# Kernel optimization log

Hardware: AMD Instinct MI355X
Metric: run time of the kernel (lower is better)

## Reference

```python
import jax, jax.numpy as jnp
import numpy as np
import math

B, S, D = 16, 2048, 64


def setup_inputs() -> dict:
    key = jax.random.key(0)
    k1, k2, k3 = jax.random.split(key, 3)
    Q = jax.random.normal(k1, (B, S, D), dtype=jnp.float32)
    K = jax.random.normal(k2, (B, S, D), dtype=jnp.float32)
    V = jax.random.normal(k3, (B, S, D), dtype=jnp.float32)
    # causal mask: True where attention is disallowed (strict upper triangle)
    mask = jnp.triu(jnp.ones((S, S), dtype=bool), k=1)
    mask = jnp.broadcast_to(mask, (B, S, S))
    return {"Q": Q, "K": K, "V": V, "mask": mask, "dk": 64}


def reference(Q, K, V, mask, dk):
    # w = Q K^T / sqrt(dk), masked fill with -1e8
    w = jnp.einsum("bqd,bkd->bqk", Q, K) / math.sqrt(dk)
    w = jnp.where(mask, jnp.float32(-1.0e8), w)
    # distance_func in the original returns 0 (constant, under no_grad),
    # so exp(-1e8 * 0) * w == w; output is softmax of masked scaled scores.
    distance_score = jnp.float32(0.0)
    s = jnp.exp(jnp.float32(-1.0e8) * distance_score) * w
    a = jax.nn.softmax(s, axis=-1)
    return a
```

## Files before the change

### kernel.cpp

```cpp
#include <hip/hip_runtime.h>

using bf16x8 = __attribute__((ext_vector_type(8))) short;
using u16x8  = __attribute__((ext_vector_type(8))) unsigned short;
using u32x4  = __attribute__((ext_vector_type(4))) unsigned;
using f32x4  = __attribute__((ext_vector_type(4))) float;

static constexpr int S  = 2048;
static constexpr int D  = 64;
static constexpr int TQ = 64;
static constexpr float QSCALE = 0.18033688f;

__device__ __forceinline__ unsigned cvtpk(float lo, float hi) {
    unsigned r;
    asm("v_cvt_pk_bf16_f32 %0, %1, %2" : "=v"(r) : "v"(lo), "v"(hi));
    return r;
}
__device__ __forceinline__ f32x4 mfma16(bf16x8 a, bf16x8 b, f32x4 c) {
    return __builtin_amdgcn_mfma_f32_16x16x32_bf16(a, b, c, 0, 0, 0);
}
__device__ __forceinline__ void lbar() {
    asm volatile("s_waitcnt lgkmcnt(0)" ::: "memory");
    __builtin_amdgcn_s_barrier();
    asm volatile("" ::: "memory");
}

__global__ __launch_bounds__(256, 2)
void monotonic_attn(const float* __restrict__ Qg, const float* __restrict__ Kg,
                    float* __restrict__ out)
{
    __shared__ unsigned short qlds[4096];
    __shared__ unsigned short kls[4][2][1024];
    __shared__ float red[4][64];

    const int bid  = blockIdx.x;
    const int xcd  = bid & 7;
    const int m    = bid >> 3;
    const int bloc = (m < 32) ? 0 : 1;
    const int qt   = (m < 32) ? (31 - m) : (m - 32);
    const int b    = 2 * xcd + bloc;

    const int tid = threadIdx.x, lane = tid & 63, wv = tid >> 6;
    const int l15 = lane & 15, g = lane >> 4;

    const float* __restrict__ Qb = Qg + (size_t)b * S * D;
    const float* __restrict__ Kb = Kg + (size_t)b * S * D;
    float* __restrict__ outb = out + (size_t)b * (size_t)S * S;

    const int q0   = qt * TQ;
    const int kend = q0 + TQ;
    const int nC   = kend >> 4;
    const int ni   = (nC - wv + 3) >> 2;

    const int srow  = lane >> 2;
    const int scp   = lane & 3;
    const int woff0 = srow * 64 + (((scp << 1)    ) ^ (srow & 7)) * 8;
    const int woff1 = srow * 64 + (((scp << 1) | 1) ^ (srow & 7)) * 8;
    const int roff0 = l15 * 64 + ((g    ) ^ (l15 & 7)) * 8;
    const int roff1 = l15 * 64 + ((4 | g) ^ (l15 & 7)) * 8;

    {
        const int qrow = tid >> 2, qc = tid & 3;
        const float4* src = reinterpret_cast<const float4*>(Qb + (size_t)(q0 + qrow) * D + qc * 16);
        float v[16];
        *reinterpret_cast<float4*>(&v[0])  = src[0];
        *reinterpret_cast<float4*>(&v[4])  = src[1];
        *reinterpret_cast<float4*>(&v[8])  = src[2];
        *reinterpret_cast<float4*>(&v[12]) = src[3];
        #pragma unroll
        for (int j = 0; j < 2; ++j) {
            u32x4 w;
            #pragma unroll
            for (int p = 0; p < 4; ++p)
                w[p] = cvtpk(v[8 * j + 2 * p] * QSCALE, v[8 * j + 2 * p + 1] * QSCALE);
            const int chunk = qc * 2 + j;
            const int off = qrow * 64 + (chunk ^ (qrow & 7)) * 8;
            *reinterpret_cast<u32x4*>(&qlds[off]) = w;
        }
    }
    lbar();

    bf16x8 qf[4][2];
    #pragma unroll
    for (int qs = 0; qs < 4; ++qs) {
        const int row = qs * 16 + l15;
        #pragma unroll
        for (int c = 0; c < 2; ++c) {
            const int off = row * 64 + ((((c << 2) | g)) ^ (row & 7)) * 8;
            qf[qs][c] = *reinterpret_cast<const bf16x8*>(&qlds[off]);
        }
    }

    float inv4[4];
    for (int pass = 0; pass < 2; ++pass) {
        float rsum[4] = {0.f, 0.f, 0.f, 0.f};

        float4 ra0, ra1, ra2, ra3, rb0, rb1, rb2, rb3;
        auto issueA = [&](int i) {
            const float4* p4 = reinterpret_cast<const float4*>(Kb) + ((wv + 4 * i) << 8) + (lane << 2);
            ra0 = p4[0]; ra1 = p4[1]; ra2 = p4[2]; ra3 = p4[3];
        };
        auto issueB = [&](int i) {
            const float4* p4 = reinterpret_cast<const float4*>(Kb) + ((wv + 4 * i) << 8) + (lane << 2);
            rb0 = p4[0]; rb1 = p4[1]; rb2 = p4[2]; rb3 = p4[3];
        };
        auto stage = [&](int i, const float4& x0, const float4& x1,
                         const float4& x2, const float4& x3) {
            u32x4 w0, w1;
            w0[0] = cvtpk(x0.x, x0.y); w0[1] = cvtpk(x0.z, x0.w);
            w0[2] = cvtpk(x1.x, x1.y); w0[3] = cvtpk(x1.z, x1.w);
            w1[0] = cvtpk(x2.x, x2.y); w1[1] = cvtpk(x2.z, x2.w);
            w1[2] = cvtpk(x3.x, x3.y); w1[3] = cvtpk(x3.z, x3.w);
            unsigned short* bp = &kls[wv][i & 1][0];
            *reinterpret_cast<u32x4*>(&bp[woff0]) = w0;
            *reinterpret_cast<u32x4*>(&bp[woff1]) = w1;
        };
        auto comp = [&](int i) {
            const unsigned short* bp = &kls[wv][i & 1][0];
            const bf16x8 kf0 = *reinterpret_cast<const bf16x8*>(&bp[roff0]);
            const bf16x8 kf1 = *reinterpret_cast<const bf16x8*>(&bp[roff1]);
            const int klo = (wv + 4 * i) << 4;
            const int kb  = klo + g * 4;
            #pragma unroll
            for (int qs = 0; qs < 4; ++qs) {
                const int qmin = q0 + qs * 16, qg = qmin + l15;
                if (pass == 0) {
                    if (klo > qmin + 15) continue;
                    f32x4 acc = {0.f, 0.f, 0.f, 0.f};
                    acc = mfma16(kf0, qf[qs][0], acc);
                    acc = mfma16(kf1, qf[qs][1], acc);
                    if (klo + 15 <= qmin) {
                        rsum[qs] += exp2f(acc[0]) + exp2f(acc[1]) + exp2f(acc[2]) + exp2f(acc[3]);
                    } else {
                        #pragma unroll
                        for (int r = 0; r < 4; ++r)
                            rsum[qs] += (kb + r <= qg) ? exp2f(acc[r]) : 0.f;
                    }
                } else {
                    f32x4 ov = {0.f, 0.f, 0.f, 0.f};
                    if (klo <= qmin + 15) {
                        f32x4 acc = {0.f, 0.f, 0.f, 0.f};
                        acc = mfma16(kf0, qf[qs][0], acc);
                        acc = mfma16(kf1, qf[qs][1], acc);
                        if (klo + 15 <= qmin) {
                            ov[0] = exp2f(acc[0]) * inv4[qs];
                            ov[1] = exp2f(acc[1]) * inv4[qs];
                            ov[2] = exp2f(acc[2]) * inv4[qs];
                            ov[3] = exp2f(acc[3]) * inv4[qs];
                        } else {
                            ov[0] = (kb + 0 <= qg) ? exp2f(acc[0]) * inv4[qs] : 0.f;
                            ov[1] = (kb + 1 <= qg) ? exp2f(acc[1]) * inv4[qs] : 0.f;
                            ov[2] = (kb + 2 <= qg) ? exp2f(acc[2]) * inv4[qs] : 0.f;
                            ov[3] = (kb + 3 <= qg) ? exp2f(acc[3]) * inv4[qs] : 0.f;
                        }
                    }
                    *reinterpret_cast<f32x4*>(outb + (size_t)qg * S + kb) = ov;
                }
            }
        };

        if (ni > 0) issueA(0);
        if (ni > 1) issueB(1);
        int i = 0;
        for (; i + 2 <= ni; i += 2) {
            stage(i, ra0, ra1, ra2, ra3);
            if (i + 2 < ni) issueA(i + 2);
            comp(i);
            stage(i + 1, rb0, rb1, rb2, rb3);
            if (i + 3 < ni) issueB(i + 3);
            comp(i + 1);
        }
        if (i < ni) { stage(i, ra0, ra1, ra2, ra3); comp(i); }

        if (pass == 0) {
            #pragma unroll
            for (int qs = 0; qs < 4; ++qs) {
                float v = rsum[qs];
                v += __shfl_xor(v, 16);
                v += __shfl_xor(v, 32);
                if (g == 0) red[wv][qs * 16 + l15] = v;
            }
            lbar();
            #pragma unroll
            for (int qs = 0; qs < 4; ++qs) {
                const int qi = qs * 16 + l15;
                inv4[qs] = 1.f / (red[0][qi] + red[1][qi] + red[2][qi] + red[3][qi]);
            }
        }
    }

    {
        f32x4 z = {0.f, 0.f, 0.f, 0.f};
        const size_t rb = (size_t)(q0 + (tid >> 2)) * S;
        for (int cc = kend + (tid & 3) * 4; cc < S; cc += 16)
            *reinterpret_cast<f32x4*>(&outb[rb + cc]) = z;
    }
}

extern "C" void kernel_launch(void* const* d_in, const int* in_sizes, int n_in,
                              void* d_out, int out_size, void* d_ws, size_t ws_size,
                              hipStream_t stream)
{
    const float* Q = (const float*)d_in[0];
    const float* K = (const float*)d_in[1];
    float* out     = (float*)d_out;
    const int nb   = in_sizes[0] / (S * D);

    monotonic_attn<<<dim3(nb * 32), dim3(256), 0, stream>>>(Q, K, out);
}
```

Measured before the change: 60.89 us.

## Pre-convert K to swizzled bf16 and stream it via global_load_lds

Adds a pre-pass kernel that converts K to bf16 once into the workspace, already in the swizzled LDS layout. The main kernel then loads K chunks straight into LDS with global_load_lds and vmcnt-based double buffering, which removes the per-block fp32 loads, conversions and LDS stores that were repeated in both passes. In exchange there is an extra kernel launch and a workspace round-trip, and the waitcnt counts are hand-tuned and must match the output stores in flight. A fallback to the old kernel remains for when no workspace is available.

After: 70.09 us. +15.1%, slower.

```diff
diff --git a/kernel.cpp b/kernel.cpp
--- a/kernel.cpp
+++ b/kernel.cpp
@@ -23,10 +23,38 @@
     __builtin_amdgcn_s_barrier();
     asm volatile("" ::: "memory");
 }
+__device__ __forceinline__ void glds16(const void* g, void* l) {
+    __builtin_amdgcn_global_load_lds(
+        (const __attribute__((address_space(1))) unsigned int*)g,
+        (__attribute__((address_space(3))) unsigned int*)l, 16, 0, 0);
+}
+#define WV0 asm volatile("s_waitcnt vmcnt(0)" ::: "memory")
+#define WV2 asm volatile("s_waitcnt vmcnt(2)" ::: "memory")
+#define WV4 asm volatile("s_waitcnt vmcnt(4)" ::: "memory")
+#define WV6 asm volatile("s_waitcnt vmcnt(6)" ::: "memory")
+
+__global__ __launch_bounds__(256)
+void conv_k(const float* __restrict__ K, unsigned short* __restrict__ ws)
+{
+    const int cid  = blockIdx.x * 4 + (threadIdx.x >> 6);
+    const int lane = threadIdx.x & 63;
+    const float4* src = reinterpret_cast<const float4*>(K + (size_t)cid * 1024 + lane * 16);
+    const float4 f0 = src[0], f1 = src[1], f2 = src[2], f3 = src[3];
+    u32x4 w0, w1;
+    w0[0] = cvtpk(f0.x, f0.y); w0[1] = cvtpk(f0.z, f0.w);
+    w0[2] = cvtpk(f1.x, f1.y); w0[3] = cvtpk(f1.z, f1.w);
+    w1[0] = cvtpk(f2.x, f2.y); w1[1] = cvtpk(f2.z, f2.w);
+    w1[2] = cvtpk(f3.x, f3.y); w1[3] = cvtpk(f3.z, f3.w);
+    const int row = lane >> 2, s = row & 7, a = lane & 3;
+    unsigned short* dst = ws + (size_t)cid * 1024;
+    *reinterpret_cast<u32x4*>(&dst[row * 64 + ((2 * a)     ^ s) * 8]) = w0;
+    *reinterpret_cast<u32x4*>(&dst[row * 64 + ((2 * a + 1) ^ s) * 8]) = w1;
+}
 
 __global__ __launch_bounds__(256, 2)
-void monotonic_attn(const float* __restrict__ Qg, const float* __restrict__ Kg,
-                    float* __restrict__ out)
+void monotonic_attn_glds(const float* __restrict__ Qg,
+                         const unsigned short* __restrict__ ws,
+                         float* __restrict__ out)
 {
     __shared__ unsigned short qlds[4096];
     __shared__ unsigned short kls[4][2][1024];
@@ -43,7 +71,7 @@
     const int l15 = lane & 15, g = lane >> 4;
 
     const float* __restrict__ Qb = Qg + (size_t)b * S * D;
-    const float* __restrict__ Kb = Kg + (size_t)b * S * D;
+    const unsigned short* __restrict__ wsb = ws + (size_t)b * 131072;
     float* __restrict__ outb = out + (size_t)b * (size_t)S * S;
 
     const int q0   = qt * TQ;
@@ -51,10 +79,6 @@
     const int nC   = kend >> 4;
     const int ni   = (nC - wv + 3) >> 2;
 
-    const int srow  = lane >> 2;
-    const int scp   = lane & 3;
-    const int woff0 = srow * 64 + (((scp << 1)    ) ^ (srow & 7)) * 8;
-    const int woff1 = srow * 64 + (((scp << 1) | 1) ^ (srow & 7)) * 8;
     const int roff0 = l15 * 64 + ((g    ) ^ (l15 & 7)) * 8;
     const int roff1 = l15 * 64 + ((4 | g) ^ (l15 & 7)) * 8;
 
@@ -90,10 +114,166 @@
         }
     }
 
+    auto glds_chunk = [&](int i) {
+        const unsigned short* gsrc = wsb + (size_t)(wv + 4 * i) * 1024 + lane * 8;
+        unsigned short* ldst = &kls[wv][i & 1][0];
+        glds16(gsrc, ldst);
+        glds16(gsrc + 512, ldst + 512);
+    };
+
+    float rsum[4] = {0.f, 0.f, 0.f, 0.f};
+    glds_chunk(0);
+    for (int i = 0; i < ni; ++i) {
+        const bool more = (i + 1 < ni);
+        if (more) { glds_chunk(i + 1); WV2; } else { WV0; }
+        const unsigned short* bp = &kls[wv][i & 1][0];
+        const bf16x8 kf0 = *reinterpret_cast<const bf16x8*>(&bp[roff0]);
+        const bf16x8 kf1 = *reinterpret_cast<const bf16x8*>(&bp[roff1]);
+        const int klo = (wv + 4 * i) << 4;
+        const int kb  = klo + g * 4;
+        #pragma unroll
+        for (int qs = 0; qs < 4; ++qs) {
+            const int qmin = q0 + qs * 16, qg = qmin + l15;
+            if (klo > qmin + 15) continue;
+            f32x4 acc = {0.f, 0.f, 0.f, 0.f};
+            acc = mfma16(kf0, qf[qs][0], acc);
+            acc = mfma16(kf1, qf[qs][1], acc);
+            if (klo + 15 <= qmin) {
+                rsum[qs] += exp2f(acc[0]) + exp2f(acc[1]) + exp2f(acc[2]) + exp2f(acc[3]);
+            } else {
+                #pragma unroll
+                for (int r = 0; r < 4; ++r)
+                    rsum[qs] += (kb + r <= qg) ? exp2f(acc[r]) : 0.f;
+            }
+        }
+    }
+    #pragma unroll
+    for (int qs = 0; qs < 4; ++qs) {
+        float v = rsum[qs];
+        v += __shfl_xor(v, 16);
+        v += __shfl_xor(v, 32);
+        if (g == 0) red[wv][qs * 16 + l15] = v;
+    }
+    lbar();
+    float inv4[4];
+    #pragma unroll
+    for (int qs = 0; qs < 4; ++qs) {
+        const int qi = qs * 16 + l15;
+        inv4[qs] = 1.f / (red[0][qi] + red[1][qi] + red[2][qi] + red[3][qi]);
+    }
+
+    glds_chunk(0);
+    for (int i = 0; i < ni; ++i) {
+        const bool more = (i + 1 < ni);
+        if (more) glds_chunk(i + 1);
+        if (i == 0) { if (more) { WV2; } else { WV0; } }
+        else        { if (more) { WV6; } else { WV4; } }
+        const unsigned short* bp = &kls[wv][i & 1][0];
+        const bf16x8 kf0 = *reinterpret_cast<const bf16x8*>(&bp[roff0]);
+        const bf16x8 kf1 = *reinterpret_cast<const bf16x8*>(&bp[roff1]);
+        const int klo = (wv + 4 * i) << 4;
+        const int kb  = klo + g * 4;
+        #pragma unroll
+        for (int qs = 0; qs < 4; ++qs) {
+            const int qmin = q0 + qs * 16, qg = qmin + l15;
+            f32x4 ov = {0.f, 0.f, 0.f, 0.f};
+            if (klo <= qmin + 15) {
+                f32x4 acc = {0.f, 0.f, 0.f, 0.f};
+                acc = mfma16(kf0, qf[qs][0], acc);
+                acc = mfma16(kf1, qf[qs][1], acc);
+                if (klo + 15 <= qmin) {
+                    ov[0] = exp2f(acc[0]) * inv4[qs];
+                    ov[1] = exp2f(acc[1]) * inv4[qs];
+                    ov[2] = exp2f(acc[2]) * inv4[qs];
+                    ov[3] = exp2f(acc[3]) * inv4[qs];
+                } else {
+                    ov[0] = (kb + 0 <= qg) ? exp2f(acc[0]) * inv4[qs] : 0.f;
+                    ov[1] = (kb + 1 <= qg) ? exp2f(acc[1]) * inv4[qs] : 0.f;
+                    ov[2] = (kb + 2 <= qg) ? exp2f(acc[2]) * inv4[qs] : 0.f;
+                    ov[3] = (kb + 3 <= qg) ? exp2f(acc[3]) * inv4[qs] : 0.f;
+                }
+            }
+            *reinterpret_cast<f32x4*>(outb + (size_t)qg * S + kb) = ov;
+        }
+    }
+
+    {
+        f32x4 z = {0.f, 0.f, 0.f, 0.f};
+        const size_t rb = (size_t)(q0 + (tid >> 2)) * S;
+        for (int cc = kend + (tid & 3) * 4; cc < S; cc += 16)
+            *reinterpret_cast<f32x4*>(&outb[rb + cc]) = z;
+    }
+}
+
+__global__ __launch_bounds__(256, 2)
+void monotonic_attn_fb(const float* __restrict__ Qg, const float* __restrict__ Kg,
+                       float* __restrict__ out)
+{
+    __shared__ unsigned short qlds[4096];
+    __shared__ unsigned short kls[4][2][1024];
+    __shared__ float red[4][64];
+
+    const int bid  = blockIdx.x;
+    const int xcd  = bid & 7;
+    const int m    = bid >> 3;
+    const int bloc = (m < 32) ? 0 : 1;
+    const int qt   = (m < 32) ? (31 - m) : (m - 32);
+    const int b    = 2 * xcd + bloc;
+
+    const int tid = threadIdx.x, lane = tid & 63, wv = tid >> 6;
+    const int l15 = lane & 15, g = lane >> 4;
+
+    const float* __restrict__ Qb = Qg + (size_t)b * S * D;
+    const float* __restrict__ Kb = Kg + (size_t)b * S * D;
+    float* __restrict__ outb = out + (size_t)b * (size_t)S * S;
+
+    const int q0   = qt * TQ;
+    const int kend = q0 + TQ;
+    const int nC   = kend >> 4;
+    const int ni   = (nC - wv + 3) >> 2;
+
+    const int srow  = lane >> 2;
+    const int scp   = lane & 3;
+    const int woff0 = srow * 64 + (((scp << 1)    ) ^ (srow & 7)) * 8;
+    const int woff1 = srow * 64 + (((scp << 1) | 1) ^ (srow & 7)) * 8;
+    const int roff0 = l15 * 64 + ((g    ) ^ (l15 & 7)) * 8;
+    const int roff1 = l15 * 64 + ((4 | g) ^ (l15 & 7)) * 8;
+
+    {
+        const int qrow = tid >> 2, qc = tid & 3;
+        const float4* src = reinterpret_cast<const float4*>(Qb + (size_t)(q0 + qrow) * D + qc * 16);
+        float v[16];
+        *reinterpret_cast<float4*>(&v[0])  = src[0];
+        *reinterpret_cast<float4*>(&v[4])  = src[1];
+        *reinterpret_cast<float4*>(&v[8])  = src[2];
+        *reinterpret_cast<float4*>(&v[12]) = src[3];
+        #pragma unroll
+        for (int j = 0; j < 2; ++j) {
+            u32x4 w;
+            #pragma unroll
+            for (int p = 0; p < 4; ++p)
+                w[p] = cvtpk(v[8 * j + 2 * p] * QSCALE, v[8 * j + 2 * p + 1] * QSCALE);
+            const int chunk = qc * 2 + j;
+            const int off = qrow * 64 + (chunk ^ (qrow & 7)) * 8;
+            *reinterpret_cast<u32x4*>(&qlds[off]) = w;
+        }
+    }
+    lbar();
+
+    bf16x8 qf[4][2];
+    #pragma unroll
+    for (int qs = 0; qs < 4; ++qs) {
+        const int row = qs * 16 + l15;
+        #pragma unroll
+        for (int c = 0; c < 2; ++c) {
+            const int off = row * 64 + ((((c << 2) | g)) ^ (row & 7)) * 8;
+            qf[qs][c] = *reinterpret_cast<const bf16x8*>(&qlds[off]);
+        }
+    }
+
     float inv4[4];
     for (int pass = 0; pass < 2; ++pass) {
         float rsum[4] = {0.f, 0.f, 0.f, 0.f};
-
         float4 ra0, ra1, ra2, ra3, rb0, rb1, rb2, rb3;
         auto issueA = [&](int i) {
             const float4* p4 = reinterpret_cast<const float4*>(Kb) + ((wv + 4 * i) << 8) + (lane << 2);
@@ -205,5 +385,12 @@
     float* out     = (float*)d_out;
     const int nb   = in_sizes[0] / (S * D);
 
-    monotonic_attn<<<dim3(nb * 32), dim3(256), 0, stream>>>(Q, K, out);
-}
+    const size_t ws_need = (size_t)nb * 128 * 1024 * sizeof(unsigned short);
+    if (d_ws != nullptr && ws_size >= ws_need) {
+        unsigned short* ws = (unsigned short*)d_ws;
+        conv_k<<<dim3(nb * 32), dim3(256), 0, stream>>>(K, ws);
+        monotonic_attn_glds<<<dim3(nb * 32), dim3(256), 0, stream>>>(Q, ws, out);
+    } else {
+        monotonic_attn_fb<<<dim3(nb * 32), dim3(256), 0, stream>>>(Q, K, out);
+    }
+}
```
